# Optimization experiments

Hardware: AMD Instinct MI355X
Metric: run time of the kernel (lower is better)

The kernel has to match this reference:

```python
import jax, jax.numpy as jnp
import numpy as np

D_MODEL = 1024
N_HEADS = 16
HEAD_DIM = D_MODEL // N_HEADS
NEG_INF = -1e30


def _rotary(v):
    # v: [B, H, T, hd]. Original module rotates each (even, odd) pair by 90 deg:
    # out[..., 2i] = -v[..., 2i+1]; out[..., 2i+1] = v[..., 2i]
    v2 = v.reshape(*v.shape[:-1], HEAD_DIM // 2, 2)
    return jnp.stack([-v2[..., 1], v2[..., 0]], axis=-1).reshape(v.shape)


def setup_inputs() -> dict:
    key = jax.random.key(0)
    ks = jax.random.split(key, 9)
    B, T, D = 2, 2048, D_MODEL
    s = 1.0 / np.sqrt(D)
    inp = {
        "x": jax.random.normal(ks[0], (B, T, D), dtype=jnp.float32),
        "Wq_w": jax.random.normal(ks[1], (D, D), dtype=jnp.float32) * s,
        "Wq_b": jnp.zeros((D,), dtype=jnp.float32),
        "Wk_w": jax.random.normal(ks[2], (D, D), dtype=jnp.float32) * s,
        "Wk_b": jnp.zeros((D,), dtype=jnp.float32),
        "Wv_w": jax.random.normal(ks[3], (D, D), dtype=jnp.float32) * s,
        "Wv_b": jnp.zeros((D,), dtype=jnp.float32),
        "Wo_w": jax.random.normal(ks[4], (D, D), dtype=jnp.float32) * s,
        "Wo_b": jnp.zeros((D,), dtype=jnp.float32),
    }
    # create_sparse_mask: block-diagonal True windows of size T//4
    window = T // 4
    blk = jnp.arange(T) // window
    inp["sparse_mask"] = blk[:, None] == blk[None, :]
    return inp


def reference(x, Wq_w, Wq_b, Wk_w, Wk_b, Wv_w, Wv_b, Wo_w, Wo_b, sparse_mask):
    B, T, D = x.shape
    H, hd = N_HEADS, HEAD_DIM

    def proj(w, b):  # [B,T,D] -> [B,H,T,hd]
        return (x @ w.T + b).reshape(B, T, H, hd).transpose(0, 2, 1, 3)

    q = _rotary(proj(Wq_w, Wq_b))
    k = _rotary(proj(Wk_w, Wk_b))
    v = proj(Wv_w, Wv_b)

    scores = jnp.einsum("bhqd,bhkd->bhqk", q, k) / jnp.sqrt(jnp.asarray(hd, x.dtype))
    causal = jnp.tril(jnp.ones((T, T), dtype=bool))
    allowed = sparse_mask & causal  # block-diagonal AND causal
    scores = jnp.where(allowed, scores, NEG_INF)
    attn = jax.nn.softmax(scores, axis=-1)  # dropout_p=0.1 omitted (eval mode)
    out = jnp.einsum("bhqk,bhkd->bhqd", attn, v)
    out = out.transpose(0, 2, 1, 3).reshape(B, T, D)
    return out @ Wo_w.T + Wo_b
```

## Files before the change

kernel.cpp:

```cpp
#include <hip/hip_runtime.h>
#include <hip/hip_bf16.h>
#include <stdint.h>

typedef __attribute__((ext_vector_type(4))) float f32x4;
typedef __attribute__((ext_vector_type(8))) __bf16 bf16x8;
typedef __attribute__((ext_vector_type(4))) unsigned short u16x4;
typedef __attribute__((ext_vector_type(8))) unsigned short u16x8;
typedef const __attribute__((address_space(1))) void* as1_cvp;
typedef __attribute__((address_space(3))) void* as3_vp;

#define LOG2E 1.44269504088896340736f

#define VMW0() asm volatile("s_waitcnt vmcnt(0)" ::: "memory")
#define VMW1() asm volatile("s_waitcnt vmcnt(1)" ::: "memory")
#define VMW2() asm volatile("s_waitcnt vmcnt(2)" ::: "memory")
#define VMW4() asm volatile("s_waitcnt vmcnt(4)" ::: "memory")
#define VMW5() asm volatile("s_waitcnt vmcnt(5)" ::: "memory")
#define VMW7() asm volatile("s_waitcnt vmcnt(7)" ::: "memory")
#define BAR()  do { __builtin_amdgcn_sched_barrier(0); __builtin_amdgcn_s_barrier(); \
                    __builtin_amdgcn_sched_barrier(0); } while (0)

static __device__ __forceinline__ unsigned short f2bf(float f) {
  union { float f; unsigned int u; } c; c.f = f;
  unsigned int r = c.u + 0x7FFFu + ((c.u >> 16) & 1u);
  return (unsigned short)(r >> 16);
}

static __device__ __forceinline__ void gl_lds16(const void* g, void* l) {
  __builtin_amdgcn_global_load_lds((as1_cvp)(uintptr_t)g, (as3_vp)(uintptr_t)l, 16, 0, 0);
}

__global__ __launch_bounds__(256) void cvt_kernel(
    const float* __restrict__ x, const float* __restrict__ wq, const float* __restrict__ wk,
    const float* __restrict__ wv, const float* __restrict__ wo,
    unsigned short* __restrict__ xb, unsigned short* __restrict__ wqb,
    unsigned short* __restrict__ wkb, unsigned short* __restrict__ wvb,
    unsigned short* __restrict__ wob) {
  long e = ((long)blockIdx.x * 256 + threadIdx.x) * 8;
  const float* s; unsigned short* d; long o;
  if (e < 4194304)      { s = x;  d = xb;  o = e; }
  else if (e < 5242880) { s = wq; d = wqb; o = e - 4194304; }
  else if (e < 6291456) { s = wk; d = wkb; o = e - 5242880; }
  else if (e < 7340032) { s = wv; d = wvb; o = e - 6291456; }
  else                  { s = wo; d = wob; o = e - 7340032; }
  float4 a = *(const float4*)(s + o);
  float4 b = *(const float4*)(s + o + 4);
  u16x8 v;
  v[0] = f2bf(a.x); v[1] = f2bf(a.y); v[2] = f2bf(a.z); v[3] = f2bf(a.w);
  v[4] = f2bf(b.x); v[5] = f2bf(b.y); v[6] = f2bf(b.z); v[7] = f2bf(b.w);
  *(u16x8*)(d + o) = v;
}

__global__ __launch_bounds__(512, 2) void gemm_qkv8(
    const unsigned short* __restrict__ xb, const unsigned short* __restrict__ wcat,
    const float* __restrict__ bq, const float* __restrict__ bk, const float* __restrict__ bv,
    unsigned short* __restrict__ qo, unsigned short* __restrict__ ko,
    unsigned short* __restrict__ vto) {
  __shared__ __align__(16) char lds[114688];
  const int tid = threadIdx.x;
  const int lane = tid & 63, wid = tid >> 6;
  const int wm = wid >> 2, wn = wid & 3;
  const int c = lane & 15, g = lane >> 4;

  const int bid = blockIdx.x;
  const int xcd = bid & 7, idx = bid >> 3;
  const int m0 = (((xcd >> 1) << 2) + (idx >> 3)) << 8;
  const int n0 = (((xcd & 1) << 3) + (idx & 7)) * 192;

  const int srow = tid >> 3;
  const int coff = (((tid & 7) ^ (srow & 7)) << 4);
  const char* Ab = (const char*)xb;
  const char* Bb = (const char*)wcat;

  const int swzr0 = ((g ^ (c & 7)) << 4);
  const int swzr1 = (((4 | g) ^ (c & 7)) << 4);

  f32x4 acc[8][3] = {};
  bf16x8 afrA[2][2], afrB[2][2], bbf[3][2];

  auto STAGE = [&](int kt, int unit) {
    char* db = lds + (kt & 1) * 57344;
    const char* gp; char* dst;
    if (unit < 3) {
      gp = Bb + ((long)(n0 + unit * 64 + srow) << 11) + (kt << 7) + coff;
      dst = db + 32768 + unit * 8192 + tid * 16;
    } else {
      const int u = unit - 3;
      gp = Ab + ((long)(m0 + u * 64 + srow) << 11) + (kt << 7) + coff;
      dst = db + u * 8192 + tid * 16;
    }
    gl_lds16(gp, dst);
  };
  auto RDA = [&](bf16x8 (&dst)[2][2], int bufb, int u) {
    const char* p = lds + bufb + (u << 13) + (((wm << 5) + c) << 7);
#pragma unroll
    for (int f = 0; f < 2; ++f) {
      dst[f][0] = *(const bf16x8*)(p + (f << 11) + swzr0);
      dst[f][1] = *(const bf16x8*)(p + (f << 11) + swzr1);
    }
  };
  auto RDB = [&](int bufb) {
#pragma unroll
    for (int nf = 0; nf < 3; ++nf) {
      const int rB = wn * 48 + (nf << 4) + c;
      const char* p = lds + bufb + 32768 + ((rB >> 6) << 13) + ((rB & 63) << 7);
      bbf[nf][0] = *(const bf16x8*)(p + swzr0);
      bbf[nf][1] = *(const bf16x8*)(p + swzr1);
    }
  };
  auto MM = [&](int u, const bf16x8 (&af)[2][2]) {
    __builtin_amdgcn_s_setprio(1);
#pragma unroll
    for (int f = 0; f < 2; ++f)
#pragma unroll
      for (int nf = 0; nf < 3; ++nf)
#pragma unroll
        for (int kf = 0; kf < 2; ++kf)
          acc[u * 2 + f][nf] = __builtin_amdgcn_mfma_f32_16x16x32_bf16(
              af[f][kf], bbf[nf][kf], acc[u * 2 + f][nf], 0, 0, 0);
    __builtin_amdgcn_s_setprio(0);
  };

#pragma unroll
  for (int uu = 0; uu < 7; ++uu) STAGE(0, uu);

#pragma unroll 1
  for (int kt = 0; kt < 15; ++kt) {
    const int bufb = (kt & 1) * 57344;
    STAGE(kt + 1, 0); STAGE(kt + 1, 1); STAGE(kt + 1, 2);
    VMW5(); BAR();
    RDB(bufb); RDA(afrA, bufb, 0); RDA(afrB, bufb, 1);
    MM(0, afrA); MM(1, afrB);
    STAGE(kt + 1, 3); STAGE(kt + 1, 4); STAGE(kt + 1, 5); STAGE(kt + 1, 6);
    VMW7(); BAR();
    RDA(afrA, bufb, 2); RDA(afrB, bufb, 3);
    MM(2, afrA); MM(3, afrB);
  }
  {
    const int bufb = 57344;
    VMW2(); BAR();
    RDB(bufb); RDA(afrA, bufb, 0); RDA(afrB, bufb, 1);
    MM(0, afrA); MM(1, afrB);
    VMW0(); BAR();
    RDA(afrA, bufb, 2); RDA(afrB, bufb, 3);
    MM(2, afrA); MM(3, afrB);
  }

#pragma unroll
  for (int nf = 0; nf < 3; ++nf) {
    const int n = n0 + wn * 48 + (nf << 4) + c;
    const int z = n >> 10, nn = n & 1023;
    const float bb_ = (z == 0 ? bq : z == 1 ? bk : bv)[nn];
    const float sc = (z == 0) ? 0.125f : 1.0f;
    const int h = nn >> 6, dd = nn & 63;
#pragma unroll
    for (int a = 0; a < 8; ++a) {
      const int mb = m0 + ((a >> 1) << 6) + (wm << 5) + ((a & 1) << 4) + (g << 2);
      const int b = mb >> 11, tt = mb & 2047;
      if (z < 2) {
        unsigned short* dst = (z == 0 ? qo : ko) +
            ((((long)(b << 4) + h) << 11) + tt) * 64 + dd;
#pragma unroll
        for (int j = 0; j < 4; ++j) dst[(long)j * 64] = f2bf((acc[a][nf][j] + bb_) * sc);
      } else {
        u16x4 pk;
#pragma unroll
        for (int j = 0; j < 4; ++j) pk[j] = f2bf(acc[a][nf][j] + bb_);
        *(u16x4*)(vto + ((((long)((b << 4) + h) << 6) + dd) << 11) + tt) = pk;
      }
    }
  }
}

__global__ __launch_bounds__(512, 2) void gemm_oproj8(
    const unsigned short* __restrict__ ab, const unsigned short* __restrict__ wob,
    const float* __restrict__ bo, float* __restrict__ out) {
  __shared__ __align__(16) char lds[65536];
  const int tid = threadIdx.x;
  const int lane = tid & 63, wid = tid >> 6;
  const int wm = wid >> 2, wn = wid & 3;
  const int c = lane & 15, g = lane >> 4;

  const int bid = blockIdx.x;
  const int swz = (bid & 7) * 32 + (bid >> 3);
  const int n0 = (swz & 7) << 7;
  const int m0 = (swz >> 3) << 7;

  const int srow = tid >> 3;
  const int coff = (((tid & 7) ^ (srow & 7)) << 4);
  const char* Ab = (const char*)ab;
  const char* Bb = (const char*)wob;

  const int swzr0 = ((g ^ (c & 7)) << 4);
  const int swzr1 = (((4 | g) ^ (c & 7)) << 4);

  f32x4 acc[4][2] = {};
  bf16x8 afrA[2][2], afrB[2][2], bbf[2][2];

  auto STAGE = [&](int kt, int unit) {
    char* db = lds + (kt & 1) * 32768;
    const char* gp;
    if (unit < 2) gp = Ab + ((long)(m0 + unit * 64 + srow) << 11) + (kt << 7) + coff;
    else          gp = Bb + ((long)(n0 + (unit - 2) * 64 + srow) << 11) + (kt << 7) + coff;
    gl_lds16(gp, db + unit * 8192 + tid * 16);
  };
  auto RDA = [&](bf16x8 (&dst)[2][2], int bufb, int u) {
    const char* p = lds + bufb + (((u << 6) + (wm << 5) + c) << 7);
#pragma unroll
    for (int f = 0; f < 2; ++f) {
      dst[f][0] = *(const bf16x8*)(p + (f << 11) + swzr0);
      dst[f][1] = *(const bf16x8*)(p + (f << 11) + swzr1);
    }
  };
  auto RDB = [&](int bufb) {
#pragma unroll
    for (int nf = 0; nf < 2; ++nf) {
      const char* p = lds + bufb + 16384 + (((nf << 6) + (wn << 4) + c) << 7);
      bbf[nf][0] = *(const bf16x8*)(p + swzr0);
      bbf[nf][1] = *(const bf16x8*)(p + swzr1);
    }
  };
  auto MM = [&](int u, const bf16x8 (&af)[2][2]) {
    __builtin_amdgcn_s_setprio(1);
#pragma unroll
    for (int f = 0; f < 2; ++f)
#pragma unroll
      for (int nf = 0; nf < 2; ++nf)
#pragma unroll
        for (int kf = 0; kf < 2; ++kf)
          acc[u * 2 + f][nf] = __builtin_amdgcn_mfma_f32_16x16x32_bf16(
              af[f][kf], bbf[nf][kf], acc[u * 2 + f][nf], 0, 0, 0);
    __builtin_amdgcn_s_setprio(0);
  };

  STAGE(0, 0); STAGE(0, 2); STAGE(0, 3); STAGE(0, 1);

#pragma unroll 1
  for (int kt = 0; kt < 15; ++kt) {
    const int bufb = (kt & 1) * 32768;
    STAGE(kt + 1, 0); STAGE(kt + 1, 2);
    VMW2(); BAR();
    RDB(bufb); RDA(afrA, bufb, 0); RDA(afrB, bufb, 1);
    MM(0, afrA);
    STAGE(kt + 1, 3); STAGE(kt + 1, 1);
    BAR();
    MM(1, afrB);
  }
  {
    VMW0(); BAR();
    RDB(32768); RDA(afrA, 32768, 0); RDA(afrB, 32768, 1);
    MM(0, afrA);
    MM(1, afrB);
  }

#pragma unroll
  for (int nf = 0; nf < 2; ++nf) {
    const int n = n0 + (nf << 6) + (wn << 4) + c;
    const float bb = bo[n];
#pragma unroll
    for (int a = 0; a < 4; ++a) {
      const int mb = m0 + ((a >> 1) << 6) + (wm << 5) + ((a & 1) << 4) + (g << 2);
#pragma unroll
      for (int j = 0; j < 4; ++j)
        out[((long)(mb + j) << 10) + n] = acc[a][nf][j] + bb;
    }
  }
}

__global__ __launch_bounds__(512) void attn_kernel(
    const unsigned short* __restrict__ qg, const unsigned short* __restrict__ kg,
    const unsigned short* __restrict__ vtg, unsigned short* __restrict__ og) {
  __shared__ __align__(16) char kv_s[3][16384];
  __shared__ __align__(16) char p_s[8][2304];

  const int bx = blockIdx.x, bh = blockIdx.y;
  const int qt = ((bx & 3) << 2) + 3 - (bx >> 2);
  const int tid = threadIdx.x;
  const int lane = tid & 63, w = tid >> 6;
  const int c = lane & 15, g = lane >> 4;
  const int q0 = qt << 7;
  const int wstart = q0 & ~511;
  const int nt = ((q0 - wstart) >> 6) + 2;

  const unsigned short* qrow = qg + (((long)bh << 11) + q0 + (w << 4) + c) * 64;
  bf16x8 qa0 = *(const bf16x8*)(qrow + (g << 3));
  bf16x8 qa1 = *(const bf16x8*)(qrow + (g << 3) + 32);

  float m_run = -3.0e38f, l_run = 0.0f;
  f32x4 oacc[4] = {};

  const int sr = tid >> 3;
  const int jx16 = (((tid & 7) ^ (sr & 7)) << 4);
  const char* kbase = (const char*)kg + ((((long)bh << 11) + sr) << 7) + jx16;
  const char* vbase = (const char*)vtg + ((((long)bh << 6) + sr) << 12) + jx16;
  const int t16 = tid << 4;

  auto STAGEKV = [&](int kv0, int bsel) {
    char* dst = kv_s[bsel];
    gl_lds16(kbase + ((long)kv0 << 7), dst + t16);
    gl_lds16(vbase + ((long)kv0 << 1), dst + 8192 + t16);
  };

  STAGEKV(wstart, 0);
  STAGEKV(wstart + 64, 1);

  int rsel = 0, ssel = 2;
  for (int t = 0; t < nt; ++t) {
    if (t + 2 < nt) {
      STAGEKV(wstart + ((t + 2) << 6), ssel);
      VMW4();
    } else if (t + 1 < nt) {
      VMW2();
    } else {
      VMW0();
    }
    BAR();

    const char* kb_ = kv_s[rsel];
    const char* vb_ = kv_s[rsel] + 8192;
    const int kv0 = wstart + (t << 6);

    f32x4 sacc[4] = {};
    __builtin_amdgcn_s_setprio(1);
#pragma unroll
    for (int mf = 0; mf < 4; ++mf) {
      const int kr = (mf << 4) + c;
      const char* kp = kb_ + (kr << 7);
      bf16x8 k0 = *(const bf16x8*)(kp + ((g ^ (kr & 7)) << 4));
      bf16x8 k1 = *(const bf16x8*)(kp + (((4 | g) ^ (kr & 7)) << 4));
      sacc[mf] = __builtin_amdgcn_mfma_f32_16x16x32_bf16(k0, qa0, sacc[mf], 0, 0, 0);
      sacc[mf] = __builtin_amdgcn_mfma_f32_16x16x32_bf16(k1, qa1, sacc[mf], 0, 0, 0);
    }
    __builtin_amdgcn_s_setprio(0);

    const int dkv = kv0 - q0;
    if (dkv > (w << 4) - 64) {
      const int qrel = (w << 4) + c;
#pragma unroll
      for (int mf = 0; mf < 4; ++mf)
#pragma unroll
        for (int j = 0; j < 4; ++j)
          if (dkv + (mf << 4) + (g << 2) + j > qrel) sacc[mf][j] = -3.0e38f;
    }

    float pmax = -3.0e38f;
#pragma unroll
    for (int mf = 0; mf < 4; ++mf)
#pragma unroll
      for (int j = 0; j < 4; ++j) pmax = fmaxf(pmax, sacc[mf][j]);
    pmax = fmaxf(pmax, __shfl_xor(pmax, 16));
    pmax = fmaxf(pmax, __shfl_xor(pmax, 32));

    const float m_new = fmaxf(m_run, pmax);
    float lsum = 0.0f;
#pragma unroll
    for (int mf = 0; mf < 4; ++mf)
#pragma unroll
      for (int j = 0; j < 4; ++j) {
        const float p = __builtin_amdgcn_exp2f((sacc[mf][j] - m_new) * LOG2E);
        sacc[mf][j] = p;
        lsum += p;
      }
    lsum += __shfl_xor(lsum, 16);
    lsum += __shfl_xor(lsum, 32);
    const float alpha = __builtin_amdgcn_exp2f((m_run - m_new) * LOG2E);
    l_run = l_run * alpha + lsum;
    m_run = m_new;

    {
      char* pw = p_s[w] + c * 144;
#pragma unroll
      for (int mf = 0; mf < 4; ++mf) {
        u16x4 pk;
#pragma unroll
        for (int j = 0; j < 4; ++j) pk[j] = f2bf(sacc[mf][j]);
        *(u16x4*)(pw + (mf << 5) + (g << 3)) = pk;
      }
    }

#pragma unroll
    for (int j = 0; j < 4; ++j) {
      const float aj = __shfl(alpha, (g << 2) + j);
#pragma unroll
      for (int nf = 0; nf < 4; ++nf) oacc[nf][j] *= aj;
    }

    const char* pr = p_s[w] + c * 144;
    __builtin_amdgcn_s_setprio(1);
#pragma unroll
    for (int kk = 0; kk < 2; ++kk) {
      bf16x8 pa = *(const bf16x8*)(pr + (kk << 6) + (g << 4));
#pragma unroll
      for (int nf = 0; nf < 4; ++nf) {
        const int vr = (nf << 4) + c;
        bf16x8 vb = *(const bf16x8*)(vb_ + (vr << 7) +
                                     ((((kk << 2) | g) ^ (vr & 7)) << 4));
        oacc[nf] = __builtin_amdgcn_mfma_f32_16x16x32_bf16(pa, vb, oacc[nf], 0, 0, 0);
      }
    }
    __builtin_amdgcn_s_setprio(0);
    BAR();

    rsel = (rsel == 2) ? 0 : rsel + 1;
    ssel = (ssel == 2) ? 0 : ssel + 1;
  }

  const int b = bh >> 4, h = bh & 15;
#pragma unroll
  for (int j = 0; j < 4; ++j) {
    const float linv = 1.0f / __shfl(l_run, (g << 2) + j);
    const int trow = q0 + (w << 4) + (g << 2) + j;
    unsigned short* dst = og + ((((long)(b << 11)) + trow) << 10) + (h << 6);
#pragma unroll
    for (int nf = 0; nf < 4; ++nf)
      dst[(nf << 4) + c] = f2bf(oacc[nf][j] * linv);
  }
}

extern "C" void kernel_launch(void* const* d_in, const int* in_sizes, int n_in,
                              void* d_out, int out_size, void* d_ws, size_t ws_size,
                              hipStream_t stream) {
  const float* x  = (const float*)d_in[0];
  const float* wq = (const float*)d_in[1];
  const float* bq = (const float*)d_in[2];
  const float* wk = (const float*)d_in[3];
  const float* bk = (const float*)d_in[4];
  const float* wv = (const float*)d_in[5];
  const float* bv = (const float*)d_in[6];
  const float* wo = (const float*)d_in[7];
  const float* bo = (const float*)d_in[8];

  char* ws = (char*)d_ws;
  unsigned short* xb    = (unsigned short*)(ws);
  unsigned short* wqb   = (unsigned short*)(ws + 8388608);
  unsigned short* wkb   = (unsigned short*)(ws + 10485760);
  unsigned short* wvb   = (unsigned short*)(ws + 12582912);
  unsigned short* wob   = (unsigned short*)(ws + 14680064);
  unsigned short* qb    = (unsigned short*)(ws + 16777216);
  unsigned short* kb    = (unsigned short*)(ws + 25165824);
  unsigned short* vtb   = (unsigned short*)(ws + 33554432);
  unsigned short* attnb = xb;

  cvt_kernel<<<4096, 256, 0, stream>>>(x, wq, wk, wv, wo, xb, wqb, wkb, wvb, wob);
  gemm_qkv8<<<256, 512, 0, stream>>>(xb, wqb, bq, bk, bv, qb, kb, vtb);
  attn_kernel<<<dim3(16, 32), 512, 0, stream>>>(qb, kb, vtb, attnb);
  gemm_oproj8<<<256, 512, 0, stream>>>(attnb, wob, bo, (float*)d_out);
}
```

Baseline: 79.54 us.

## Retile QKV GEMM warps and add lazy softmax rescaling in attention

The QKV projection GEMM changes its warp layout from 2x4 to 4x2, so each warp computes a 64x96 tile. The old split-stage pipeline with partial vmcnt waits becomes one full-tile loop per k-step that issues all loads for the next stage, then waits on vmcnt(0). This raises fragment reuse per LDS read but drops the finer overlap between loads and MFMAs. The attention kernel now skips the output and row-sum rescale when the new block max stays within a threshold of the running max, removing exp and shuffle work on most iterations.

```diff
diff --git a/kernel.cpp b/kernel.cpp
--- a/kernel.cpp
+++ b/kernel.cpp
@@ -12,11 +12,8 @@
 #define LOG2E 1.44269504088896340736f
 
 #define VMW0() asm volatile("s_waitcnt vmcnt(0)" ::: "memory")
-#define VMW1() asm volatile("s_waitcnt vmcnt(1)" ::: "memory")
 #define VMW2() asm volatile("s_waitcnt vmcnt(2)" ::: "memory")
 #define VMW4() asm volatile("s_waitcnt vmcnt(4)" ::: "memory")
-#define VMW5() asm volatile("s_waitcnt vmcnt(5)" ::: "memory")
-#define VMW7() asm volatile("s_waitcnt vmcnt(7)" ::: "memory")
 #define BAR()  do { __builtin_amdgcn_sched_barrier(0); __builtin_amdgcn_s_barrier(); \
                     __builtin_amdgcn_sched_barrier(0); } while (0)
 
@@ -59,7 +56,7 @@
   __shared__ __align__(16) char lds[114688];
   const int tid = threadIdx.x;
   const int lane = tid & 63, wid = tid >> 6;
-  const int wm = wid >> 2, wn = wid & 3;
+  const int wm = wid >> 1, wn = wid & 1;
   const int c = lane & 15, g = lane >> 4;
 
   const int bid = blockIdx.x;
@@ -75,8 +72,7 @@
   const int swzr0 = ((g ^ (c & 7)) << 4);
   const int swzr1 = (((4 | g) ^ (c & 7)) << 4);
 
-  f32x4 acc[8][3] = {};
-  bf16x8 afrA[2][2], afrB[2][2], bbf[3][2];
+  f32x4 acc[4][6] = {};
 
   auto STAGE = [&](int kt, int unit) {
     char* db = lds + (kt & 1) * 57344;
@@ -91,71 +87,55 @@
     }
     gl_lds16(gp, dst);
   };
-  auto RDA = [&](bf16x8 (&dst)[2][2], int bufb, int u) {
-    const char* p = lds + bufb + (u << 13) + (((wm << 5) + c) << 7);
-#pragma unroll
-    for (int f = 0; f < 2; ++f) {
-      dst[f][0] = *(const bf16x8*)(p + (f << 11) + swzr0);
-      dst[f][1] = *(const bf16x8*)(p + (f << 11) + swzr1);
-    }
-  };
-  auto RDB = [&](int bufb) {
-#pragma unroll
-    for (int nf = 0; nf < 3; ++nf) {
-      const int rB = wn * 48 + (nf << 4) + c;
-      const char* p = lds + bufb + 32768 + ((rB >> 6) << 13) + ((rB & 63) << 7);
-      bbf[nf][0] = *(const bf16x8*)(p + swzr0);
-      bbf[nf][1] = *(const bf16x8*)(p + swzr1);
-    }
-  };
-  auto MM = [&](int u, const bf16x8 (&af)[2][2]) {
-    __builtin_amdgcn_s_setprio(1);
-#pragma unroll
-    for (int f = 0; f < 2; ++f)
-#pragma unroll
-      for (int nf = 0; nf < 3; ++nf)
-#pragma unroll
-        for (int kf = 0; kf < 2; ++kf)
-          acc[u * 2 + f][nf] = __builtin_amdgcn_mfma_f32_16x16x32_bf16(
-              af[f][kf], bbf[nf][kf], acc[u * 2 + f][nf], 0, 0, 0);
-    __builtin_amdgcn_s_setprio(0);
-  };
 
 #pragma unroll
   for (int uu = 0; uu < 7; ++uu) STAGE(0, uu);
+  VMW0();
+  BAR();
 
 #pragma unroll 1
-  for (int kt = 0; kt < 15; ++kt) {
+  for (int kt = 0; kt < 16; ++kt) {
     const int bufb = (kt & 1) * 57344;
-    STAGE(kt + 1, 0); STAGE(kt + 1, 1); STAGE(kt + 1, 2);
-    VMW5(); BAR();
-    RDB(bufb); RDA(afrA, bufb, 0); RDA(afrB, bufb, 1);
-    MM(0, afrA); MM(1, afrB);
-    STAGE(kt + 1, 3); STAGE(kt + 1, 4); STAGE(kt + 1, 5); STAGE(kt + 1, 6);
-    VMW7(); BAR();
-    RDA(afrA, bufb, 2); RDA(afrB, bufb, 3);
-    MM(2, afrA); MM(3, afrB);
-  }
-  {
-    const int bufb = 57344;
-    VMW2(); BAR();
-    RDB(bufb); RDA(afrA, bufb, 0); RDA(afrB, bufb, 1);
-    MM(0, afrA); MM(1, afrB);
-    VMW0(); BAR();
-    RDA(afrA, bufb, 2); RDA(afrB, bufb, 3);
-    MM(2, afrA); MM(3, afrB);
-  }
-
-#pragma unroll
-  for (int nf = 0; nf < 3; ++nf) {
-    const int n = n0 + wn * 48 + (nf << 4) + c;
+    if (kt < 15) {
+#pragma unroll
+      for (int uu = 0; uu < 7; ++uu) STAGE(kt + 1, uu);
+    }
+    bf16x8 aa[4][2];
+    const char* pA = lds + bufb + (wm << 13) + (c << 7);
+#pragma unroll
+    for (int f = 0; f < 4; ++f) {
+      aa[f][0] = *(const bf16x8*)(pA + (f << 11) + swzr0);
+      aa[f][1] = *(const bf16x8*)(pA + (f << 11) + swzr1);
+    }
+#pragma unroll
+    for (int nf = 0; nf < 6; ++nf) {
+      const int rB = wn * 96 + (nf << 4) + c;
+      const char* pB = lds + bufb + 32768 + ((rB >> 6) << 13) + ((rB & 63) << 7);
+      bf16x8 b0 = *(const bf16x8*)(pB + swzr0);
+      bf16x8 b1 = *(const bf16x8*)(pB + swzr1);
+      __builtin_amdgcn_s_setprio(1);
+#pragma unroll
+      for (int f = 0; f < 4; ++f)
+        acc[f][nf] = __builtin_amdgcn_mfma_f32_16x16x32_bf16(aa[f][0], b0, acc[f][nf], 0, 0, 0);
+#pragma unroll
+      for (int f = 0; f < 4; ++f)
+        acc[f][nf] = __builtin_amdgcn_mfma_f32_16x16x32_bf16(aa[f][1], b1, acc[f][nf], 0, 0, 0);
+      __builtin_amdgcn_s_setprio(0);
+    }
+    if (kt < 15) VMW0();
+    BAR();
+  }
+
+#pragma unroll
+  for (int nf = 0; nf < 6; ++nf) {
+    const int n = n0 + wn * 96 + (nf << 4) + c;
     const int z = n >> 10, nn = n & 1023;
     const float bb_ = (z == 0 ? bq : z == 1 ? bk : bv)[nn];
     const float sc = (z == 0) ? 0.125f : 1.0f;
     const int h = nn >> 6, dd = nn & 63;
 #pragma unroll
-    for (int a = 0; a < 8; ++a) {
-      const int mb = m0 + ((a >> 1) << 6) + (wm << 5) + ((a & 1) << 4) + (g << 2);
+    for (int a = 0; a < 4; ++a) {
+      const int mb = m0 + (wm << 6) + (a << 4) + (g << 2);
       const int b = mb >> 11, tt = mb & 2047;
       if (z < 2) {
         unsigned short* dst = (z == 0 ? qo : ko) +
@@ -351,7 +331,9 @@
     pmax = fmaxf(pmax, __shfl_xor(pmax, 16));
     pmax = fmaxf(pmax, __shfl_xor(pmax, 32));
 
-    const float m_new = fmaxf(m_run, pmax);
+    const bool resc = !__all(pmax <= m_run + 8.0f);
+    const float m_new = resc ? fmaxf(m_run, pmax) : m_run;
+
     float lsum = 0.0f;
 #pragma unroll
     for (int mf = 0; mf < 4; ++mf)
@@ -363,9 +345,19 @@
       }
     lsum += __shfl_xor(lsum, 16);
     lsum += __shfl_xor(lsum, 32);
-    const float alpha = __builtin_amdgcn_exp2f((m_run - m_new) * LOG2E);
-    l_run = l_run * alpha + lsum;
-    m_run = m_new;
+
+    if (resc) {
+      const float alpha = __builtin_amdgcn_exp2f((m_run - m_new) * LOG2E);
+      l_run *= alpha;
+#pragma unroll
+      for (int j = 0; j < 4; ++j) {
+        const float aj = __shfl(alpha, (g << 2) + j);
+#pragma unroll
+        for (int nf = 0; nf < 4; ++nf) oacc[nf][j] *= aj;
+      }
+      m_run = m_new;
+    }
+    l_run += lsum;
 
     {
       char* pw = p_s[w] + c * 144;
@@ -376,13 +368,6 @@
         for (int j = 0; j < 4; ++j) pk[j] = f2bf(sacc[mf][j]);
         *(u16x4*)(pw + (mf << 5) + (g << 3)) = pk;
       }
-    }
-
-#pragma unroll
-    for (int j = 0; j < 4; ++j) {
-      const float aj = __shfl(alpha, (g << 2) + j);
-#pragma unroll
-      for (int nf = 0; nf < 4; ++nf) oacc[nf][j] *= aj;
     }
 
     const char* pr = p_s[w] + c * 144;
```

Measured after the change: 79.01 us. No clear change (-0.7%).
